# Performance work log

Hardware: AMD Instinct MI355X
Metric: run time of the kernel (lower is better)

Reference implementation:

```python
import jax, jax.numpy as jnp
import numpy as np

D_MODEL = 768
NUM_HEADS = 12
D_K = D_MODEL // NUM_HEADS


def setup_inputs() -> dict:
    key = jax.random.key(0)
    ks = jax.random.split(key, 11)
    B, S, D = 2, 4096, D_MODEL
    s = 1.0 / np.sqrt(D)
    return {
        "query": jax.random.normal(ks[0], (B, S, D), jnp.float32),
        "key": jax.random.normal(ks[1], (B, S, D), jnp.float32),
        "value": jax.random.normal(ks[2], (B, S, D), jnp.float32),
        "Wq": jax.random.normal(ks[3], (D, D), jnp.float32) * s,
        "bq": jnp.zeros((D,), jnp.float32),
        "Wk": jax.random.normal(ks[4], (D, D), jnp.float32) * s,
        "bk": jnp.zeros((D,), jnp.float32),
        "Wv": jax.random.normal(ks[5], (D, D), jnp.float32) * s,
        "bv": jnp.zeros((D,), jnp.float32),
        "Wo": jax.random.normal(ks[6], (D, D), jnp.float32) * s,
        "bo": jnp.zeros((D,), jnp.float32),
    }


def reference(query, key, value, Wq, bq, Wk, bk, Wv, bv, Wo, bo):
    B, S, D = query.shape
    H, dk = NUM_HEADS, D_K
    # torch Linear: y = x @ W^T + b
    def proj(x, W, b):
        return (x @ W.T + b).reshape(B, S, H, dk).transpose(0, 2, 1, 3)  # [B,H,S,dk]
    q = proj(query, Wq, bq)
    k = proj(key, Wk, bk)
    v = proj(value, Wv, bv)
    scores = jnp.einsum("bhqd,bhkd->bhqk", q, k) / jnp.sqrt(jnp.float32(dk))
    attn = jax.nn.softmax(scores, axis=-1)  # dropout is identity in eval mode
    x = jnp.einsum("bhqk,bhkd->bhqd", attn, v)
    x = x.transpose(0, 2, 1, 3).reshape(B, S, D)
    return x @ Wo.T + bo
```

## Files before the change

### kernel.cpp

```cpp
#include <hip/hip_runtime.h>
#include <hip/hip_bf16.h>


typedef __attribute__((ext_vector_type(8))) short short8;
typedef __attribute__((ext_vector_type(4))) float floatx4;
typedef __attribute__((ext_vector_type(4))) float float4v;

#define S_LEN 4096
#define D_MODEL 768
#define NUM_HEADS 12
#define DK 64
#define BATCH 2
#define M_ROWS (BATCH * S_LEN)
#define HEADS_TOTAL (BATCH * NUM_HEADS)
#define QSCALE 0.1803368801111204f

__device__ __forceinline__ unsigned short f2bf(float f) {
    union { float f; unsigned int i; } v; v.f = f;
    unsigned int r = v.i + 0x7fff + ((v.i >> 16) & 1);
    return (unsigned short)(r >> 16);
}

__device__ __forceinline__ unsigned int cvt_pk_bf16(float a, float b) {
    unsigned int r;
    asm("v_cvt_pk_bf16_f32 %0, %1, %2" : "=v"(r) : "v"(a), "v"(b));
    return r;
}

__device__ __forceinline__ float exp2_fast(float x) {
    float r;
    asm("v_exp_f32 %0, %1" : "=v"(r) : "v"(x));
    return r;
}

__device__ __forceinline__ int swz(int r, int c) {
    return (r << 6) + ((((c >> 3) ^ (r & 7)) << 3) | (c & 7));
}

__device__ __forceinline__ void pack8(const float4v& f0, const float4v& f1,
                                      unsigned short* __restrict__ dst) {
    uint4 w;
    w.x = cvt_pk_bf16(f0[0], f0[1]);
    w.y = cvt_pk_bf16(f0[2], f0[3]);
    w.z = cvt_pk_bf16(f1[0], f1[1]);
    w.w = cvt_pk_bf16(f1[2], f1[3]);
    *(uint4*)dst = w;
}

template <int MODE, int XF32>
__global__ __launch_bounds__(256, 6) void gemm_bt(
    const void* __restrict__ Xv,
    const float* __restrict__ W,
    const float* __restrict__ bias,
    void* __restrict__ outv,
    int M, int N, int K)
{
    __shared__ __align__(16) unsigned short As[64][72];
    __shared__ __align__(16) unsigned short Bs[64][72];

    const int t    = threadIdx.x;
    const int wv   = t >> 6;
    const int lane = t & 63;
    const int l15  = lane & 15;
    const int quad = lane >> 4;
    const int m0   = blockIdx.x * 64;
    const int n0   = blockIdx.y * 64;

    floatx4 acc[4];
#pragma unroll
    for (int i = 0; i < 4; ++i) acc[i] = (floatx4){0.f, 0.f, 0.f, 0.f};

    const int srow = t >> 3;
    const int scol = (t & 7) * 8;

    float4v xf0, xf1, xf2, xf3;
    uint4   xu0, xu1;
    float4v wf0, wf1, wf2, wf3;

#define G_LOAD(k0)                                                                      \
    do {                                                                                \
        if (XF32) {                                                                     \
            const float* xp = (const float*)Xv + (long)(m0 + srow) * K + (k0) + scol;   \
            xf0 = *(const float4v*)xp; xf1 = *(const float4v*)(xp + 4);                 \
            xp += (long)32 * K;                                                         \
            xf2 = *(const float4v*)xp; xf3 = *(const float4v*)(xp + 4);                 \
        } else {                                                                        \
            const unsigned short* xp =                                                  \
                (const unsigned short*)Xv + (long)(m0 + srow) * K + (k0) + scol;        \
            xu0 = *(const uint4*)xp;                                                    \
            xu1 = *(const uint4*)(xp + (long)32 * K);                                   \
        }                                                                               \
        const float* wp = W + (long)(n0 + srow) * K + (k0) + scol;                      \
        wf0 = *(const float4v*)wp; wf1 = *(const float4v*)(wp + 4);                     \
        wp += (long)32 * K;                                                             \
        wf2 = *(const float4v*)wp; wf3 = *(const float4v*)(wp + 4);                     \
    } while (0)

#define G_WRITE()                                                                       \
    do {                                                                                \
        if (XF32) {                                                                     \
            pack8(xf0, xf1, &As[srow][scol]);                                           \
            pack8(xf2, xf3, &As[32 + srow][scol]);                                      \
        } else {                                                                        \
            *(uint4*)(&As[srow][scol]) = xu0;                                           \
            *(uint4*)(&As[32 + srow][scol]) = xu1;                                      \
        }                                                                               \
        pack8(wf0, wf1, &Bs[srow][scol]);                                               \
        pack8(wf2, wf3, &Bs[32 + srow][scol]);                                          \
    } while (0)

    G_LOAD(0);
    G_WRITE();
    __syncthreads();

    for (int k0 = 0; k0 < K; k0 += 64) {
        const bool more = (k0 + 64 < K);
        if (more) G_LOAD(k0 + 64);
#pragma unroll
        for (int kk = 0; kk < 2; ++kk) {
            short8 a = *(const short8*)(&As[wv * 16 + l15][kk * 32 + quad * 8]);
#pragma unroll
            for (int nj = 0; nj < 4; ++nj) {
                short8 b = *(const short8*)(&Bs[nj * 16 + l15][kk * 32 + quad * 8]);
                acc[nj] = __builtin_amdgcn_mfma_f32_16x16x32_bf16(a, b, acc[nj], 0, 0, 0);
            }
        }
        __syncthreads();
        if (more) G_WRITE();
        __syncthreads();
    }
#undef G_LOAD
#undef G_WRITE

    if (MODE == 2) {
#pragma unroll
        for (int nj = 0; nj < 4; ++nj) {
            const float bv = bias[n0 + nj * 16 + l15];
#pragma unroll
            for (int reg = 0; reg < 4; ++reg) {
                const int row = wv * 16 + quad * 4 + reg;
                const int col = nj * 16 + l15;
                As[row][col ^ (((row >> 3) & 7) << 3)] = f2bf(acc[nj][reg] + bv);
            }
        }
        __syncthreads();
        const int bb = m0 >> 12;
        const int hh = n0 >> 6;
        const int sl = (m0 & 4095) + scol;
        const int c  = t & 7;
#pragma unroll
        for (int p = 0; p < 2; ++p) {
            const int d = p * 32 + srow;
            const int colp = d ^ (c << 3);
            unsigned short w[8];
#pragma unroll
            for (int j = 0; j < 8; ++j) w[j] = As[scol + j][colp];
            unsigned short* outp = (unsigned short*)outv +
                ((long)((bb * NUM_HEADS + hh) * DK + d)) * S_LEN + sl;
            *(uint4*)outp = *(uint4*)w;
        }
        return;
    }

#pragma unroll
    for (int nj = 0; nj < 4; ++nj) {
        const int col = n0 + nj * 16 + l15;
        const float bv = bias[col];
#pragma unroll
        for (int reg = 0; reg < 4; ++reg) {
            const int row = m0 + wv * 16 + quad * 4 + reg;
            const float o = acc[nj][reg] + bv;
            if (MODE == 0) {
                ((float*)outv)[(long)row * N + col] = o;
            } else {
                const int bb = row >> 12;
                const int ss = row & 4095;
                const int h  = col >> 6;
                const int d  = col & 63;
                ((unsigned short*)outv)[(((long)bb * NUM_HEADS + h) * S_LEN + ss) * DK + d] = f2bf(o);
            }
        }
    }
}

__global__ __launch_bounds__(256, 6) void flash_attn_fused(
    const float* __restrict__ Xq,
    const float* __restrict__ Wq,
    const float* __restrict__ bq,
    const unsigned short* __restrict__ Kg,
    const unsigned short* __restrict__ VTg,
    unsigned short* __restrict__ ctx)
{
    __shared__ __align__(16) unsigned short Ks[4096];
    __shared__ __align__(16) unsigned short Vt[4096];
    __shared__ __align__(16) unsigned short Pq[4096];

    const int t    = threadIdx.x;
    const int wv   = t >> 6;
    const int lane = t & 63;
    const int l15  = lane & 15;
    const int quad = lane >> 4;
    const int q0   = blockIdx.x * 64;
    const int bh   = blockIdx.y;
    const int bb   = bh / NUM_HEADS;
    const int h    = bh % NUM_HEADS;
    const long kbase = (long)bh * S_LEN * DK;
    const long vbase = (long)bh * DK * S_LEN;

    const int srow = t >> 3;
    const int scol = (t & 7) * 8;

    const int st_a = swz(srow, scol);
    const int st_b = swz(32 + srow, scol);
    int frag_row[4];
#pragma unroll
    for (int nj = 0; nj < 4; ++nj) frag_row[nj] = swz(nj * 16 + l15, quad * 8);

    {
        floatx4 qacc[4];
#pragma unroll
        for (int i = 0; i < 4; ++i) qacc[i] = (floatx4){0.f, 0.f, 0.f, 0.f};

        for (int k0 = 0; k0 < D_MODEL; k0 += 64) {
            {
                const float* xp = Xq + ((long)bb * S_LEN + q0 + srow) * D_MODEL + k0 + scol;
                float4v a0 = *(const float4v*)xp, a1 = *(const float4v*)(xp + 4);
                const float* xp2 = xp + (long)32 * D_MODEL;
                float4v a2 = *(const float4v*)xp2, a3 = *(const float4v*)(xp2 + 4);
                const float* wp = Wq + (long)(h * DK + srow) * D_MODEL + k0 + scol;
                float4v b0 = *(const float4v*)wp, b1 = *(const float4v*)(wp + 4);
                const float* wp2 = wp + (long)32 * D_MODEL;
                float4v b2 = *(const float4v*)wp2, b3 = *(const float4v*)(wp2 + 4);
                pack8(a0, a1, &Ks[st_a]); pack8(a2, a3, &Ks[st_b]);
                pack8(b0, b1, &Vt[st_a]); pack8(b2, b3, &Vt[st_b]);
            }
            __syncthreads();
#pragma unroll
            for (int kk = 0; kk < 2; ++kk) {
                short8 a = *(const short8*)(&Ks[swz(wv * 16 + l15, kk * 32 + quad * 8)]);
#pragma unroll
                for (int nj = 0; nj < 4; ++nj) {
                    short8 b = *(const short8*)(&Vt[swz(nj * 16 + l15, kk * 32 + quad * 8)]);
                    qacc[nj] = __builtin_amdgcn_mfma_f32_16x16x32_bf16(a, b, qacc[nj], 0, 0, 0);
                }
            }
            __syncthreads();
        }
#pragma unroll
        for (int nj = 0; nj < 4; ++nj) {
            const float bv = bq[h * DK + nj * 16 + l15];
#pragma unroll
            for (int reg = 0; reg < 4; ++reg) {
                const int row = wv * 16 + quad * 4 + reg;
                Pq[swz(row, nj * 16 + l15)] = f2bf((qacc[nj][reg] + bv) * QSCALE);
            }
        }
    }

    uint4 kr0 = *(const uint4*)(Kg + kbase + (long)srow * DK + scol);
    uint4 kr1 = *(const uint4*)(Kg + kbase + (long)(32 + srow) * DK + scol);
    uint4 vr0 = *(const uint4*)(VTg + vbase + (long)srow * S_LEN + scol);
    uint4 vr1 = *(const uint4*)(VTg + vbase + (long)(32 + srow) * S_LEN + scol);

    asm volatile("s_waitcnt lgkmcnt(0)" ::: "memory");
    short8 qfrag[2];
#pragma unroll
    for (int kk = 0; kk < 2; ++kk)
        qfrag[kk] = *(const short8*)(&Pq[swz(wv * 16 + l15, kk * 32 + quad * 8)]);

    *(uint4*)(&Ks[st_a]) = kr0; *(uint4*)(&Ks[st_b]) = kr1;
    *(uint4*)(&Vt[st_a]) = vr0; *(uint4*)(&Vt[st_b]) = vr1;
    __syncthreads();

    float l_loc = 0.f;
    floatx4 acc[4];
#pragma unroll
    for (int i = 0; i < 4; ++i) acc[i] = (floatx4){0.f, 0.f, 0.f, 0.f};

    const unsigned short* kp = Kg + kbase + (long)64 * DK;
    const unsigned short* vp = VTg + vbase + 64;
    const int pw0 = swz(wv * 16 + l15, quad * 4);

    for (int tix = 0; tix < 64; ++tix) {
        if (tix < 63) {
            kr0 = *(const uint4*)(kp + (long)srow * DK + scol);
            kr1 = *(const uint4*)(kp + (long)(32 + srow) * DK + scol);
            vr0 = *(const uint4*)(vp + (long)srow * S_LEN + scol);
            vr1 = *(const uint4*)(vp + (long)(32 + srow) * S_LEN + scol);
            kp += (long)64 * DK;
            vp += 64;
        }

        floatx4 sc[4];
#pragma unroll
        for (int i = 0; i < 4; ++i) sc[i] = (floatx4){0.f, 0.f, 0.f, 0.f};
        __builtin_amdgcn_s_setprio(1);
#pragma unroll
        for (int kk = 0; kk < 2; ++kk) {
#pragma unroll
            for (int nj = 0; nj < 4; ++nj) {
                short8 kf = *(const short8*)(&Ks[frag_row[nj] + ((kk * 4) ^ 0) * 0 + swz(0, kk * 32) ]);
                kf = *(const short8*)(&Ks[swz(nj * 16 + l15, kk * 32 + quad * 8)]);
                sc[nj] = __builtin_amdgcn_mfma_f32_16x16x32_bf16(kf, qfrag[kk], sc[nj], 0, 0, 0);
            }
        }
        __builtin_amdgcn_s_setprio(0);

#pragma unroll
        for (int nj = 0; nj < 4; ++nj) {
            const float e0 = exp2_fast(sc[nj][0]);
            const float e1 = exp2_fast(sc[nj][1]);
            const float e2 = exp2_fast(sc[nj][2]);
            const float e3 = exp2_fast(sc[nj][3]);
            l_loc += (e0 + e1) + (e2 + e3);
            uint2 w;
            w.x = cvt_pk_bf16(e0, e1);
            w.y = cvt_pk_bf16(e2, e3);
            *(uint2*)(&Pq[swz(wv * 16 + l15, nj * 16 + quad * 4)]) = w;
        }
        asm volatile("s_waitcnt lgkmcnt(0)" ::: "memory");

        __builtin_amdgcn_s_setprio(1);
#pragma unroll
        for (int kk = 0; kk < 2; ++kk) {
            short8 a = *(const short8*)(&Pq[swz(wv * 16 + l15, kk * 32 + quad * 8)]);
#pragma unroll
            for (int dj = 0; dj < 4; ++dj) {
                short8 b = *(const short8*)(&Vt[swz(dj * 16 + l15, kk * 32 + quad * 8)]);
                acc[dj] = __builtin_amdgcn_mfma_f32_16x16x32_bf16(a, b, acc[dj], 0, 0, 0);
            }
        }
        __builtin_amdgcn_s_setprio(0);

        __syncthreads();
        if (tix < 63) {
            *(uint4*)(&Ks[st_a]) = kr0; *(uint4*)(&Ks[st_b]) = kr1;
            *(uint4*)(&Vt[st_a]) = vr0; *(uint4*)(&Vt[st_b]) = vr1;
        }
        __syncthreads();
    }

    float l_full = l_loc;
    l_full += __shfl_xor(l_full, 16);
    l_full += __shfl_xor(l_full, 32);
    float l_row[4];
#pragma unroll
    for (int reg = 0; reg < 4; ++reg)
        l_row[reg] = __shfl(l_full, quad * 4 + reg);
#pragma unroll
    for (int dj = 0; dj < 4; ++dj) {
#pragma unroll
        for (int reg = 0; reg < 4; ++reg) {
            const int ss = q0 + wv * 16 + quad * 4 + reg;
            const float v = acc[dj][reg] / l_row[reg];
            ctx[((long)bb * S_LEN + ss) * D_MODEL + h * DK + dj * 16 + l15] = f2bf(v);
        }
    }
}

__global__ void fill_sentinel(float* out, long n, float val) {
    long i = (long)blockIdx.x * blockDim.x + threadIdx.x;
    if (i < n) out[i] = val;
}

extern "C" void kernel_launch(void* const* d_in, const int* in_sizes, int n_in,
                              void* d_out, int out_size, void* d_ws, size_t ws_size,
                              hipStream_t stream)
{
    const float* q_in = (const float*)d_in[0];
    const float* k_in = (const float*)d_in[1];
    const float* v_in = (const float*)d_in[2];
    const float* Wq = (const float*)d_in[3];
    const float* bq = (const float*)d_in[4];
    const float* Wk = (const float*)d_in[5];
    const float* bk = (const float*)d_in[6];
    const float* Wv = (const float*)d_in[7];
    const float* bv = (const float*)d_in[8];
    const float* Wo = (const float*)d_in[9];
    const float* bo = (const float*)d_in[10];

    const long NELEM = (long)M_ROWS * D_MODEL;
    const size_t needed = (size_t)(3 * NELEM) * sizeof(unsigned short);

    if (ws_size < needed) {
        const long n = (long)out_size;
        fill_sentinel<<<(n + 255) / 256, 256, 0, stream>>>((float*)d_out, n,
                                                           (float)(ws_size >> 20));
        return;
    }

    unsigned short* ws  = (unsigned short*)d_ws;
    unsigned short* kp  = ws;
    unsigned short* vtp = ws + NELEM;
    unsigned short* ctx = ws + 2 * NELEM;

    dim3 ggrid(M_ROWS / 64, D_MODEL / 64);
    gemm_bt<1, 1><<<ggrid, 256, 0, stream>>>(k_in, Wk, bk, kp, M_ROWS, D_MODEL, D_MODEL);
    gemm_bt<2, 1><<<ggrid, 256, 0, stream>>>(v_in, Wv, bv, vtp, M_ROWS, D_MODEL, D_MODEL);

    dim3 agrid(S_LEN / 64, HEADS_TOTAL);
    flash_attn_fused<<<agrid, 256, 0, stream>>>(q_in, Wq, bq, kp, vtp, ctx);

    gemm_bt<0, 0><<<ggrid, 256, 0, stream>>>(ctx, Wo, bo, d_out, M_ROWS, D_MODEL, D_MODEL);
}
```

Before: 387.7 us.

## Enlarge GEMM tiles to 128x128 with double-buffered swizzled LDS and block remap

The projection GEMM moves from 64x64 tiles (one 16-row strip per wave) to 128x128 tiles where each wave computes a 64x64 sub-tile with a 4x4 accumulator grid. It double-buffers the swizzled LDS tiles and prefetches two steps ahead to cut barriers and raise MFMA-to-load ratio. It also remaps block ids for L2 locality and rewrites the transposed-V epilogue. Cost: many more registers (launch bounds drop to 2 blocks/CU) and only 384 blocks per GEMM, which lowers occupancy and wave-level parallelism. Dead code in the attention kernel is removed.

Result: slower. 402.3 us (+3.8%).

```diff
diff --git a/kernel.cpp b/kernel.cpp
--- a/kernel.cpp
+++ b/kernel.cpp
@@ -48,138 +48,169 @@
 }
 
 template <int MODE, int XF32>
-__global__ __launch_bounds__(256, 6) void gemm_bt(
+__global__ __launch_bounds__(256, 2) void gemm_bt(
     const void* __restrict__ Xv,
     const float* __restrict__ W,
     const float* __restrict__ bias,
     void* __restrict__ outv,
     int M, int N, int K)
 {
-    __shared__ __align__(16) unsigned short As[64][72];
-    __shared__ __align__(16) unsigned short Bs[64][72];
+    __shared__ __align__(16) unsigned short As[2][8192];
+    __shared__ __align__(16) unsigned short Bs[2][8192];
 
     const int t    = threadIdx.x;
     const int wv   = t >> 6;
     const int lane = t & 63;
     const int l15  = lane & 15;
     const int quad = lane >> 4;
-    const int m0   = blockIdx.x * 64;
-    const int n0   = blockIdx.y * 64;
-
-    floatx4 acc[4];
-#pragma unroll
-    for (int i = 0; i < 4; ++i) acc[i] = (floatx4){0.f, 0.f, 0.f, 0.f};
-
-    const int srow = t >> 3;
+    const int wm   = wv >> 1;
+    const int wn   = wv & 1;
+
+    const int bid = blockIdx.y * gridDim.x + blockIdx.x;
+    const int wg  = (bid & 7) * 48 + (bid >> 3);
+    const int m0  = (wg / 6) * 128;
+    const int n0  = (wg % 6) * 128;
+
+    floatx4 acc[4][4];
+#pragma unroll
+    for (int i = 0; i < 4; ++i)
+#pragma unroll
+        for (int j = 0; j < 4; ++j) acc[i][j] = (floatx4){0.f, 0.f, 0.f, 0.f};
+
+    const int sr   = t >> 3;
     const int scol = (t & 7) * 8;
-
-    float4v xf0, xf1, xf2, xf3;
-    uint4   xu0, xu1;
-    float4v wf0, wf1, wf2, wf3;
-
-#define G_LOAD(k0)                                                                      \
-    do {                                                                                \
-        if (XF32) {                                                                     \
-            const float* xp = (const float*)Xv + (long)(m0 + srow) * K + (k0) + scol;   \
-            xf0 = *(const float4v*)xp; xf1 = *(const float4v*)(xp + 4);                 \
-            xp += (long)32 * K;                                                         \
-            xf2 = *(const float4v*)xp; xf3 = *(const float4v*)(xp + 4);                 \
-        } else {                                                                        \
-            const unsigned short* xp =                                                  \
-                (const unsigned short*)Xv + (long)(m0 + srow) * K + (k0) + scol;        \
-            xu0 = *(const uint4*)xp;                                                    \
-            xu1 = *(const uint4*)(xp + (long)32 * K);                                   \
-        }                                                                               \
-        const float* wp = W + (long)(n0 + srow) * K + (k0) + scol;                      \
-        wf0 = *(const float4v*)wp; wf1 = *(const float4v*)(wp + 4);                     \
-        wp += (long)32 * K;                                                             \
-        wf2 = *(const float4v*)wp; wf3 = *(const float4v*)(wp + 4);                     \
+    const int st0  = swz(sr, scol);
+
+    float4v xa[8];
+    uint4   xu[4];
+    float4v wa[8];
+
+#define G_LOAD(step)                                                                     \
+    do {                                                                                 \
+        const long kofs = (long)(step) * 64;                                             \
+        _Pragma("unroll")                                                                \
+        for (int p = 0; p < 4; ++p) {                                                    \
+            if (XF32) {                                                                  \
+                const float* xp = (const float*)Xv + (long)(m0 + sr + 32 * p) * K + kofs + scol; \
+                xa[2 * p]     = *(const float4v*)xp;                                     \
+                xa[2 * p + 1] = *(const float4v*)(xp + 4);                               \
+            } else {                                                                     \
+                const unsigned short* xp =                                               \
+                    (const unsigned short*)Xv + (long)(m0 + sr + 32 * p) * K + kofs + scol; \
+                xu[p] = *(const uint4*)xp;                                               \
+            }                                                                            \
+            const float* wp = W + (long)(n0 + sr + 32 * p) * K + kofs + scol;            \
+            wa[2 * p]     = *(const float4v*)wp;                                         \
+            wa[2 * p + 1] = *(const float4v*)(wp + 4);                                   \
+        }                                                                                \
     } while (0)
 
-#define G_WRITE()                                                                       \
-    do {                                                                                \
-        if (XF32) {                                                                     \
-            pack8(xf0, xf1, &As[srow][scol]);                                           \
-            pack8(xf2, xf3, &As[32 + srow][scol]);                                      \
-        } else {                                                                        \
-            *(uint4*)(&As[srow][scol]) = xu0;                                           \
-            *(uint4*)(&As[32 + srow][scol]) = xu1;                                      \
-        }                                                                               \
-        pack8(wf0, wf1, &Bs[srow][scol]);                                               \
-        pack8(wf2, wf3, &Bs[32 + srow][scol]);                                          \
+#define G_WRITE(buf)                                                                     \
+    do {                                                                                 \
+        _Pragma("unroll")                                                                \
+        for (int p = 0; p < 4; ++p) {                                                    \
+            if (XF32) pack8(xa[2 * p], xa[2 * p + 1], &As[buf][st0 + p * 2048]);         \
+            else      *(uint4*)(&As[buf][st0 + p * 2048]) = xu[p];                       \
+            pack8(wa[2 * p], wa[2 * p + 1], &Bs[buf][st0 + p * 2048]);                   \
+        }                                                                                \
     } while (0)
 
+    const int NS = K / 64;
     G_LOAD(0);
-    G_WRITE();
+    G_WRITE(0);
+    G_LOAD(1);
     __syncthreads();
 
-    for (int k0 = 0; k0 < K; k0 += 64) {
-        const bool more = (k0 + 64 < K);
-        if (more) G_LOAD(k0 + 64);
+    int cur = 0;
+    for (int s = 0; s < NS; ++s) {
+        const unsigned short* Ab = &As[cur][0];
+        const unsigned short* Bb = &Bs[cur][0];
 #pragma unroll
         for (int kk = 0; kk < 2; ++kk) {
-            short8 a = *(const short8*)(&As[wv * 16 + l15][kk * 32 + quad * 8]);
+            short8 af[4];
+#pragma unroll
+            for (int mi = 0; mi < 4; ++mi)
+                af[mi] = *(const short8*)(Ab + swz(wm * 64 + mi * 16 + l15, kk * 32 + quad * 8));
 #pragma unroll
             for (int nj = 0; nj < 4; ++nj) {
-                short8 b = *(const short8*)(&Bs[nj * 16 + l15][kk * 32 + quad * 8]);
-                acc[nj] = __builtin_amdgcn_mfma_f32_16x16x32_bf16(a, b, acc[nj], 0, 0, 0);
-            }
-        }
-        __syncthreads();
-        if (more) G_WRITE();
-        __syncthreads();
+                short8 bf = *(const short8*)(Bb + swz(wn * 64 + nj * 16 + l15, kk * 32 + quad * 8));
+#pragma unroll
+                for (int mi = 0; mi < 4; ++mi)
+                    acc[mi][nj] = __builtin_amdgcn_mfma_f32_16x16x32_bf16(af[mi], bf, acc[mi][nj], 0, 0, 0);
+            }
+        }
+        if (s + 1 < NS) {
+            G_WRITE(cur ^ 1);
+            if (s + 2 < NS) G_LOAD(s + 2);
+            __syncthreads();
+            cur ^= 1;
+        }
     }
 #undef G_LOAD
 #undef G_WRITE
 
     if (MODE == 2) {
-#pragma unroll
-        for (int nj = 0; nj < 4; ++nj) {
-            const float bv = bias[n0 + nj * 16 + l15];
+        unsigned short* Sx = &As[0][0];
+        const int bb2 = m0 >> 12;
+        const int h0  = n0 >> 6;
+        const int slb = m0 & 4095;
+        __syncthreads();
+#pragma unroll
+        for (int hx = 0; hx < 2; ++hx) {
+            if (wn == hx) {
+#pragma unroll
+                for (int nj = 0; nj < 4; ++nj) {
+                    const float bvv = bias[n0 + hx * 64 + nj * 16 + l15];
+                    const int col = nj * 16 + l15;
+#pragma unroll
+                    for (int mi = 0; mi < 4; ++mi)
+#pragma unroll
+                        for (int reg = 0; reg < 4; ++reg) {
+                            const int row = wm * 64 + mi * 16 + quad * 4 + reg;
+                            Sx[(row << 6) + (col ^ ((row & 7) << 3))] =
+                                f2bf(acc[mi][nj][reg] + bvv);
+                        }
+                }
+            }
+            __syncthreads();
+#pragma unroll
+            for (int p = 0; p < 4; ++p) {
+                const int ci = t + (p << 8);
+                const int d  = ci >> 4;
+                const int s0 = (ci & 15) << 3;
+                unsigned short w[8];
+#pragma unroll
+                for (int j = 0; j < 8; ++j)
+                    w[j] = Sx[((s0 + j) << 6) + (d ^ (j << 3))];
+                unsigned short* outp = (unsigned short*)outv +
+                    ((long)((bb2 * NUM_HEADS + h0 + hx) * DK + d)) * S_LEN + slb + s0;
+                *(uint4*)outp = *(uint4*)w;
+            }
+            __syncthreads();
+        }
+        return;
+    }
+
+#pragma unroll
+    for (int nj = 0; nj < 4; ++nj) {
+        const int col = n0 + wn * 64 + nj * 16 + l15;
+        const float bv = bias[col];
+#pragma unroll
+        for (int mi = 0; mi < 4; ++mi)
 #pragma unroll
             for (int reg = 0; reg < 4; ++reg) {
-                const int row = wv * 16 + quad * 4 + reg;
-                const int col = nj * 16 + l15;
-                As[row][col ^ (((row >> 3) & 7) << 3)] = f2bf(acc[nj][reg] + bv);
-            }
-        }
-        __syncthreads();
-        const int bb = m0 >> 12;
-        const int hh = n0 >> 6;
-        const int sl = (m0 & 4095) + scol;
-        const int c  = t & 7;
-#pragma unroll
-        for (int p = 0; p < 2; ++p) {
-            const int d = p * 32 + srow;
-            const int colp = d ^ (c << 3);
-            unsigned short w[8];
-#pragma unroll
-            for (int j = 0; j < 8; ++j) w[j] = As[scol + j][colp];
-            unsigned short* outp = (unsigned short*)outv +
-                ((long)((bb * NUM_HEADS + hh) * DK + d)) * S_LEN + sl;
-            *(uint4*)outp = *(uint4*)w;
-        }
-        return;
-    }
-
-#pragma unroll
-    for (int nj = 0; nj < 4; ++nj) {
-        const int col = n0 + nj * 16 + l15;
-        const float bv = bias[col];
-#pragma unroll
-        for (int reg = 0; reg < 4; ++reg) {
-            const int row = m0 + wv * 16 + quad * 4 + reg;
-            const float o = acc[nj][reg] + bv;
-            if (MODE == 0) {
-                ((float*)outv)[(long)row * N + col] = o;
-            } else {
-                const int bb = row >> 12;
-                const int ss = row & 4095;
-                const int h  = col >> 6;
-                const int d  = col & 63;
-                ((unsigned short*)outv)[(((long)bb * NUM_HEADS + h) * S_LEN + ss) * DK + d] = f2bf(o);
-            }
-        }
+                const int row = m0 + wm * 64 + mi * 16 + quad * 4 + reg;
+                const float o = acc[mi][nj][reg] + bv;
+                if (MODE == 0) {
+                    ((float*)outv)[(long)row * N + col] = o;
+                } else {
+                    const int bb = row >> 12;
+                    const int ss = row & 4095;
+                    const int h  = col >> 6;
+                    const int d  = col & 63;
+                    ((unsigned short*)outv)[(((long)bb * NUM_HEADS + h) * S_LEN + ss) * DK + d] = f2bf(o);
+                }
+            }
     }
 }
 
@@ -212,9 +243,6 @@
 
     const int st_a = swz(srow, scol);
     const int st_b = swz(32 + srow, scol);
-    int frag_row[4];
-#pragma unroll
-    for (int nj = 0; nj < 4; ++nj) frag_row[nj] = swz(nj * 16 + l15, quad * 8);
 
     {
         floatx4 qacc[4];
@@ -279,7 +307,6 @@
 
     const unsigned short* kp = Kg + kbase + (long)64 * DK;
     const unsigned short* vp = VTg + vbase + 64;
-    const int pw0 = swz(wv * 16 + l15, quad * 4);
 
     for (int tix = 0; tix < 64; ++tix) {
         if (tix < 63) {
@@ -299,8 +326,7 @@
         for (int kk = 0; kk < 2; ++kk) {
 #pragma unroll
             for (int nj = 0; nj < 4; ++nj) {
-                short8 kf = *(const short8*)(&Ks[frag_row[nj] + ((kk * 4) ^ 0) * 0 + swz(0, kk * 32) ]);
-                kf = *(const short8*)(&Ks[swz(nj * 16 + l15, kk * 32 + quad * 8)]);
+                short8 kf = *(const short8*)(&Ks[swz(nj * 16 + l15, kk * 32 + quad * 8)]);
                 sc[nj] = __builtin_amdgcn_mfma_f32_16x16x32_bf16(kf, qfrag[kk], sc[nj], 0, 0, 0);
             }
         }
@@ -394,7 +420,7 @@
     unsigned short* vtp = ws + NELEM;
     unsigned short* ctx = ws + 2 * NELEM;
 
-    dim3 ggrid(M_ROWS / 64, D_MODEL / 64);
+    dim3 ggrid(M_ROWS / 128, D_MODEL / 128);
     gemm_bt<1, 1><<<ggrid, 256, 0, stream>>>(k_in, Wk, bk, kp, M_ROWS, D_MODEL, D_MODEL);
     gemm_bt<2, 1><<<ggrid, 256, 0, stream>>>(v_in, Wv, bv, vtp, M_ROWS, D_MODEL, D_MODEL);
 
```
